# Optimization experiments

Measured on AMD Instinct MI355X. Metric: run time of the kernel, lower is better.

The kernel has to match this reference:

```python
import jax, jax.numpy as jnp
import numpy as np

N, NFEAT, NHID, NREL, NCLASS, NHEADS = 4096, 512, 64, 64, 16, 8
ALPHA = 0.2   # LeakyReLU negative slope
NEG = -9e15   # pyGAT mask value


def _gat_layer(x, rel, mask, adj_ad, W, a1, a2, concat):
    # x: [N, Fin], rel: [nrel, Fin], mask: [N, N] bool, adj_ad: [N, nrel]
    xr = x + adj_ad @ rel                 # relation-augmented node features
    h = xr @ W                            # [N, Fout]
    f1 = h @ a1                           # [N]  (a^T[Wh_i||Wh_j] = f1_i + f2_j)
    f2 = h @ a2                           # [N]
    e = jax.nn.leaky_relu(f1[:, None] + f2[None, :], ALPHA)  # [N, N]
    att = jax.nn.softmax(jnp.where(mask, e, NEG), axis=1)
    out = att @ h                         # [N, Fout]
    return jax.nn.elu(out) if concat else out


def setup_inputs() -> dict:
    key = jax.random.key(0)
    ks = jax.random.split(key, 12)
    x = jax.random.normal(ks[0], (N, NFEAT), jnp.float32)
    rel = jax.random.normal(ks[1], (NREL, NFEAT), jnp.float32)
    rel_dict = jax.random.randint(ks[2], (N,), 0, NREL, jnp.int32)
    adj = (jax.random.uniform(ks[3], (N, N)) < 0.01).astype(jnp.float32)
    adj = jnp.maximum(adj, jnp.eye(N, dtype=jnp.float32))  # self loops
    adj_ad = jax.random.uniform(ks[4], (N, NREL), jnp.float32)
    adj_ad = adj_ad / adj_ad.sum(axis=1, keepdims=True)
    s_in = 1.0 / np.sqrt(NFEAT)
    s_hid = 1.0 / np.sqrt(NHID)
    s_cat = 1.0 / np.sqrt(NHID * NHEADS)
    W_heads = jax.random.normal(ks[5], (NHEADS, NFEAT, NHID), jnp.float32) * s_in
    a1_heads = jax.random.normal(ks[6], (NHEADS, NHID), jnp.float32) * s_hid
    a2_heads = jax.random.normal(ks[7], (NHEADS, NHID), jnp.float32) * s_hid
    W_out = jax.random.normal(ks[8], (NHID * NHEADS, NFEAT), jnp.float32) * s_cat
    a1_out = jax.random.normal(ks[9], (NFEAT,), jnp.float32) * s_in
    a2_out = jax.random.normal(ks[10], (NFEAT,), jnp.float32) * s_in
    lin_W = jax.random.normal(ks[11], (NFEAT, NCLASS), jnp.float32) * s_in
    lin_b = jnp.zeros((NCLASS,), jnp.float32)
    return {"x": x, "rel": rel, "rel_dict": rel_dict, "adj": adj, "adj_ad": adj_ad,
            "W_heads": W_heads, "a1_heads": a1_heads, "a2_heads": a2_heads,
            "W_out": W_out, "a1_out": a1_out, "a2_out": a2_out,
            "lin_W": lin_W, "lin_b": lin_b}


def reference(x, rel, rel_dict, adj, adj_ad, W_heads, a1_heads, a2_heads,
              W_out, a1_out, a2_out, lin_W, lin_b):
    # dropout is identity at inference (training=False); rel_dict is only used
    # by the repo to build adj/adj_ad, so it is a non-math constant here.
    mask = adj > 0
    # multi-head GAT layer, heads fused via vmap then concatenated on feature dim
    heads = jax.vmap(lambda W, a1, a2: _gat_layer(x, rel, mask, adj_ad, W, a1, a2, True))(
        W_heads, a1_heads, a2_heads)                      # [H, N, NHID]
    hcat = jnp.moveaxis(heads, 0, 1).reshape(N, NHEADS * NHID)  # [N, H*NHID]
    h2 = _gat_layer(hcat, rel, mask, adj_ad, W_out, a1_out, a2_out, False)  # [N, NFEAT]
    logits = jax.nn.elu(h2 @ lin_W + lin_b)               # [N, NCLASS]
    return jax.nn.log_softmax(logits, axis=1)
```

## Files before the change

kernel.cpp:

```cpp
#include <hip/hip_runtime.h>

#define NN      4096
#define FEAT    512
#define NHID    64
#define NHEADS  8
#define NCLS    16
#define MAXDEG  128
#define ALPHA   0.2f

typedef __bf16 bf16_t;
typedef __bf16 bf16x8_t __attribute__((ext_vector_type(8)));
typedef float  f32x4_t  __attribute__((ext_vector_type(4)));
typedef unsigned short us8_t __attribute__((ext_vector_type(8)));

__device__ inline unsigned short f2bf(float f) {
    unsigned int u = __float_as_uint(f);
    u += 0x7fffu + ((u >> 16) & 1u);
    return (unsigned short)(u >> 16);
}
__device__ inline float bfu2f(unsigned short b) {
    return __uint_as_float(((unsigned int)b) << 16);
}

__global__ __launch_bounds__(128) void rmmfuse_kernel(
    const float* __restrict__ adj_ad, const float* __restrict__ rel,
    const float* __restrict__ x, float* __restrict__ R,
    bf16_t* __restrict__ Abf) {
    int i = blockIdx.x;
    int t = threadIdx.x;
    __shared__ float sa[64];
    if (t < 64) sa[t] = adj_ad[i * 64 + t];
    __syncthreads();
    float4 acc = make_float4(0.f, 0.f, 0.f, 0.f);
    for (int r = 0; r < 64; ++r) {
        float a = sa[r];
        float4 rv = ((const float4*)(rel + r * FEAT))[t];
        acc.x += a * rv.x; acc.y += a * rv.y;
        acc.z += a * rv.z; acc.w += a * rv.w;
    }
    ((float4*)(R + (size_t)i * FEAT))[t] = acc;
    float4 xv = ((const float4*)(x + (size_t)i * FEAT))[t];
    ushort4 o;
    o.x = f2bf(acc.x + xv.x); o.y = f2bf(acc.y + xv.y);
    o.z = f2bf(acc.z + xv.z); o.w = f2bf(acc.w + xv.w);
    *(ushort4*)(Abf + (size_t)i * FEAT + 4 * t) = o;
}

__global__ __launch_bounds__(256) void wperm_kernel(
    const float* __restrict__ Wh, const float* __restrict__ Wo,
    unsigned short* __restrict__ WcT, unsigned short* __restrict__ WoT) {
    int gid = blockIdx.x * 256 + threadIdx.x;
    if (gid < 262144) {
        int idx = gid;
        int n = idx >> 9, k = idx & 511;
        int h = n >> 6, f = n & 63;
        WcT[idx] = f2bf(Wh[(h * 512 + k) * 64 + f]);
    } else {
        int idx = gid - 262144;
        int n = idx >> 9, k = idx & 511;
        WoT[idx] = f2bf(Wo[k * 512 + n]);
    }
}

__global__ __launch_bounds__(256) void gemm_bf16_dot_kernel(
    const bf16_t* __restrict__ A, const bf16_t* __restrict__ Bt,
    unsigned short* __restrict__ Cbf,
    const float* __restrict__ a1, const float* __restrict__ a2,
    float* __restrict__ f1, float* __restrict__ f2, int layer2) {
    __shared__ __align__(16) bf16_t As[64][72];
    __shared__ __align__(16) bf16_t Bs[64][72];
    const int bm = blockIdx.x * 64;
    const int bn = blockIdx.y * 64;
    const int t  = threadIdx.x;
    const int lr = t >> 3;
    const int lc = (t & 7) * 8;
    const int l  = t & 63;
    const int w  = t >> 6;
    const int mrow = w * 16 + (l & 15);
    const int nrow = l & 15;
    const int q8 = (l >> 4) * 8;

    f32x4_t acc[4] = {};
    for (int k0 = 0; k0 < FEAT; k0 += 64) {
        *(uint4*)&As[lr][lc]      = *(const uint4*)(A  + (size_t)(bm + lr)      * FEAT + k0 + lc);
        *(uint4*)&As[32 + lr][lc] = *(const uint4*)(A  + (size_t)(bm + 32 + lr) * FEAT + k0 + lc);
        *(uint4*)&Bs[lr][lc]      = *(const uint4*)(Bt + (size_t)(bn + lr)      * FEAT + k0 + lc);
        *(uint4*)&Bs[32 + lr][lc] = *(const uint4*)(Bt + (size_t)(bn + 32 + lr) * FEAT + k0 + lc);
        __syncthreads();
        #pragma unroll
        for (int kk = 0; kk < 64; kk += 32) {
            bf16x8_t a = *(const bf16x8_t*)&As[mrow][kk + q8];
            #pragma unroll
            for (int nt = 0; nt < 4; ++nt) {
                bf16x8_t b = *(const bf16x8_t*)&Bs[nt * 16 + nrow][kk + q8];
                acc[nt] = __builtin_amdgcn_mfma_f32_16x16x32_bf16(a, b, acc[nt], 0, 0, 0);
            }
        }
        __syncthreads();
    }
    const int crow = bm + w * 16 + (l >> 4) * 4;
    const int ccol = bn + (l & 15);
    #pragma unroll
    for (int nt = 0; nt < 4; ++nt)
        #pragma unroll
        for (int r = 0; r < 4; ++r)
            Cbf[(size_t)(crow + r) * FEAT + ccol + nt * 16] = f2bf(acc[nt][r]);

    float a1v[4], a2v[4];
    #pragma unroll
    for (int nt = 0; nt < 4; ++nt) {
        a1v[nt] = a1[bn + (l & 15) + nt * 16];
        a2v[nt] = a2[bn + (l & 15) + nt * 16];
    }
    float p1[4] = {}, p2[4] = {};
    #pragma unroll
    for (int nt = 0; nt < 4; ++nt)
        #pragma unroll
        for (int r = 0; r < 4; ++r) {
            p1[r] += acc[nt][r] * a1v[nt];
            p2[r] += acc[nt][r] * a2v[nt];
        }
    #pragma unroll
    for (int off = 1; off <= 8; off <<= 1)
        #pragma unroll
        for (int r = 0; r < 4; ++r) {
            p1[r] += __shfl_xor(p1[r], off);
            p2[r] += __shfl_xor(p2[r], off);
        }
    if ((l & 15) == 0) {
        int row = bm + w * 16 + (l >> 4) * 4;
        if (layer2) {
            #pragma unroll
            for (int r = 0; r < 4; ++r) {
                atomicAdd(&f1[row + r], p1[r]);
                atomicAdd(&f2[row + r], p2[r]);
            }
        } else {
            #pragma unroll
            for (int r = 0; r < 4; ++r) {
                f1[blockIdx.y * NN + row + r] = p1[r];
                f2[blockIdx.y * NN + row + r] = p2[r];
            }
        }
    }
}

__global__ __launch_bounds__(256) void initf_kernel(float* __restrict__ f1o,
                                                    float* __restrict__ f2o) {
    int idx = blockIdx.x * 256 + threadIdx.x;
    ((float4*)f1o)[idx] = make_float4(0.f, 0.f, 0.f, 0.f);
    ((float4*)f2o)[idx] = make_float4(0.f, 0.f, 0.f, 0.f);
}

__device__ inline void csr_emit(unsigned long long m, int lane, int* cnt,
                                int* colrow, int j) {
    if (m) {
        int tot = __popcll(m);
        int base = 0;
        if (lane == 0) base = atomicAdd(cnt, tot);
        base = __shfl(base, 0);
        if (m & (1ULL << lane)) {
            int pos = __popcll(m & ((1ULL << lane) - 1));
            int idx = base + pos;
            if (idx < MAXDEG) colrow[idx] = j;
        }
    }
}
__global__ __launch_bounds__(256) void csr_kernel(
    const float* __restrict__ adj, int* __restrict__ deg, int* __restrict__ cols) {
    int i = blockIdx.x;
    int t = threadIdx.x;
    int lane = t & 63;
    __shared__ int cnt;
    if (t == 0) cnt = 0;
    __syncthreads();
    const float4* row4 = (const float4*)(adj + (size_t)i * NN);
    int* colrow = cols + i * MAXDEG;
    for (int j4 = t; j4 < NN / 4; j4 += 256) {
        float4 v = row4[j4];
        int j = j4 * 4;
        csr_emit(__ballot(v.x > 0.0f), lane, &cnt, colrow, j);
        csr_emit(__ballot(v.y > 0.0f), lane, &cnt, colrow, j + 1);
        csr_emit(__ballot(v.z > 0.0f), lane, &cnt, colrow, j + 2);
        csr_emit(__ballot(v.w > 0.0f), lane, &cnt, colrow, j + 3);
    }
    __syncthreads();
    if (t == 0) deg[i] = cnt > MAXDEG ? MAXDEG : cnt;
}

__global__ __launch_bounds__(512) void att1_kernel(
    const bf16_t* __restrict__ Hbf, const float* __restrict__ f1,
    const float* __restrict__ f2, const int* __restrict__ deg,
    const int* __restrict__ cols, const float* __restrict__ R,
    bf16_t* __restrict__ outbf) {
    int i = blockIdx.x;
    int h = threadIdx.x >> 6;
    int l = threadIdx.x & 63;
    __shared__ int jl[MAXDEG];
    __shared__ float se[NHEADS][MAXDEG];
    __shared__ int sdeg;
    if (threadIdx.x == 0) sdeg = deg[i];
    __syncthreads();
    int d = sdeg;
    int dpad = (d + 15) & ~15;
    for (int k = threadIdx.x; k < dpad; k += 512)
        jl[k] = (k < d) ? cols[i * MAXDEG + k] : i;
    __syncthreads();
    float fi = f1[h * NN + i];
    float lmax = -1e30f;
    for (int k = l; k < d; k += 64) {
        float e = fi + f2[h * NN + jl[k]];
        e = e > 0.0f ? e : ALPHA * e;
        se[h][k] = e;
        lmax = fmaxf(lmax, e);
    }
    for (int off = 32; off; off >>= 1) lmax = fmaxf(lmax, __shfl_down(lmax, off));
    float m = __shfl(lmax, 0);
    float ls = 0.0f;
    for (int k = l; k < d; k += 64) {
        float p = __expf(se[h][k] - m);
        se[h][k] = p;
        ls += p;
    }
    for (int k = d + l; k < dpad; k += 64) se[h][k] = 0.0f;
    for (int off = 32; off; off >>= 1) ls += __shfl_down(ls, off);
    float s = __shfl(ls, 0);
    const int slot = l >> 3;
    const int cg   = l & 7;
    float acc[8] = {};
    for (int k0 = 0; k0 < dpad; k0 += 16) {
        int ka = k0 + slot;
        int kb = k0 + 8 + slot;
        float pa = se[h][ka];
        us8_t va = *(const us8_t*)(Hbf + (size_t)jl[ka] * FEAT + h * 64 + cg * 8);
        float pb = (kb < dpad) ? se[h][kb] : 0.0f;
        us8_t vb = (kb < dpad) ? *(const us8_t*)(Hbf + (size_t)jl[kb] * FEAT + h * 64 + cg * 8)
                               : va;
        #pragma unroll
        for (int j = 0; j < 8; ++j) acc[j] += pa * bfu2f(va[j]);
        #pragma unroll
        for (int j = 0; j < 8; ++j) acc[j] += pb * bfu2f(vb[j]);
    }
    #pragma unroll
    for (int off = 8; off <= 32; off <<= 1)
        #pragma unroll
        for (int j = 0; j < 8; ++j) acc[j] += __shfl_xor(acc[j], off);
    if (slot == 0) {
        float inv = 1.0f / s;
        const float* Rrow = R + (size_t)i * FEAT + h * 64 + cg * 8;
        float4 r0 = *(const float4*)(Rrow);
        float4 r1 = *(const float4*)(Rrow + 4);
        float o[8];
        #pragma unroll
        for (int j = 0; j < 8; ++j) {
            float v = acc[j] * inv;
            o[j] = v > 0.0f ? v : __expf(v) - 1.0f;
        }
        o[0] += r0.x; o[1] += r0.y; o[2] += r0.z; o[3] += r0.w;
        o[4] += r1.x; o[5] += r1.y; o[6] += r1.z; o[7] += r1.w;
        ushort4 pk0, pk1;
        pk0.x = f2bf(o[0]); pk0.y = f2bf(o[1]); pk0.z = f2bf(o[2]); pk0.w = f2bf(o[3]);
        pk1.x = f2bf(o[4]); pk1.y = f2bf(o[5]); pk1.z = f2bf(o[6]); pk1.w = f2bf(o[7]);
        ushort4* dst = (ushort4*)(outbf + (size_t)i * FEAT + h * 64 + cg * 8);
        dst[0] = pk0;
        dst[1] = pk1;
    }
}

__global__ __launch_bounds__(256) void att2_final_kernel(
    const bf16_t* __restrict__ Hbf, const float* __restrict__ f1,
    const float* __restrict__ f2, const int* __restrict__ deg,
    const int* __restrict__ cols, const float* __restrict__ linW,
    const float* __restrict__ linb, float* __restrict__ out) {
    int i = blockIdx.x;
    int t = threadIdx.x;
    __shared__ int jl[MAXDEG];
    __shared__ float sp[MAXDEG];
    __shared__ float red[4];
    __shared__ float part[3][FEAT];
    __shared__ float hrow[FEAT];
    __shared__ float clsred[16][NCLS];
    __shared__ float sl[NCLS];
    __shared__ int sdeg;
    if (t == 0) sdeg = deg[i];
    __syncthreads();
    int d = sdeg;
    int dpad = (d + 7) & ~7;
    if (t < dpad) jl[t] = (t < d) ? cols[i * MAXDEG + t] : i;
    __syncthreads();
    float e = 0.0f, lmax = -1e30f;
    if (t < d) {
        e = f1[i] + f2[jl[t]];
        e = e > 0.0f ? e : ALPHA * e;
        lmax = e;
    }
    for (int off = 32; off; off >>= 1) lmax = fmaxf(lmax, __shfl_down(lmax, off));
    if ((t & 63) == 0) red[t >> 6] = lmax;
    __syncthreads();
    float m = fmaxf(fmaxf(red[0], red[1]), fmaxf(red[2], red[3]));
    float p = 0.0f;
    if (t < d) p = __expf(e - m);
    if (t < dpad) sp[t] = p;
    float ls = p;
    for (int off = 32; off; off >>= 1) ls += __shfl_down(ls, off);
    __syncthreads();
    if ((t & 63) == 0) red[t >> 6] = ls;
    __syncthreads();
    float s = red[0] + red[1] + red[2] + red[3];
    float inv = 1.0f / s;
    const int slot = t >> 6;
    const int cg   = t & 63;
    float acc[8] = {};
    for (int k0 = 0; k0 < dpad; k0 += 8) {
        int ka = k0 + slot;
        int kb = k0 + 4 + slot;
        float pa = sp[ka];
        us8_t va = *(const us8_t*)(Hbf + (size_t)jl[ka] * FEAT + cg * 8);
        float pb = (kb < dpad) ? sp[kb] : 0.0f;
        us8_t vb = (kb < dpad) ? *(const us8_t*)(Hbf + (size_t)jl[kb] * FEAT + cg * 8) : va;
        #pragma unroll
        for (int j = 0; j < 8; ++j) acc[j] += pa * bfu2f(va[j]);
        #pragma unroll
        for (int j = 0; j < 8; ++j) acc[j] += pb * bfu2f(vb[j]);
    }
    if (slot > 0) {
        float* dst = &part[slot - 1][cg * 8];
        *(float4*)(dst)     = make_float4(acc[0], acc[1], acc[2], acc[3]);
        *(float4*)(dst + 4) = make_float4(acc[4], acc[5], acc[6], acc[7]);
    }
    __syncthreads();
    if (slot == 0) {
        #pragma unroll
        for (int sl2 = 0; sl2 < 3; ++sl2)
            #pragma unroll
            for (int j = 0; j < 8; ++j) acc[j] += part[sl2][cg * 8 + j];
        float* dst = &hrow[cg * 8];
        *(float4*)(dst)     = make_float4(acc[0] * inv, acc[1] * inv, acc[2] * inv, acc[3] * inv);
        *(float4*)(dst + 4) = make_float4(acc[4] * inv, acc[5] * inv, acc[6] * inv, acc[7] * inv);
    }
    __syncthreads();
    {
        int c = t & 15;
        int seg = t >> 4;
        float partial = 0.0f;
        int f0 = seg * 32;
        #pragma unroll 8
        for (int f = f0; f < f0 + 32; ++f) partial += hrow[f] * linW[f * NCLS + c];
        clsred[seg][c] = partial;
    }
    __syncthreads();
    if (t < NCLS) {
        float logit = linb[t];
        #pragma unroll
        for (int seg = 0; seg < 16; ++seg) logit += clsred[seg][t];
        logit = logit > 0.0f ? logit : __expf(logit) - 1.0f;
        sl[t] = logit;
    }
    __syncthreads();
    if (t < NCLS) {
        float mm = sl[0];
        #pragma unroll
        for (int c = 1; c < NCLS; ++c) mm = fmaxf(mm, sl[c]);
        float ssum = 0.0f;
        #pragma unroll
        for (int c = 0; c < NCLS; ++c) ssum += __expf(sl[c] - mm);
        out[i * NCLS + t] = sl[t] - mm - logf(ssum);
    }
}

extern "C" void kernel_launch(void* const* d_in, const int* in_sizes, int n_in,
                              void* d_out, int out_size, void* d_ws, size_t ws_size,
                              hipStream_t stream) {
    const float* x        = (const float*)d_in[0];
    const float* rel      = (const float*)d_in[1];
    const float* adj      = (const float*)d_in[3];
    const float* adj_ad   = (const float*)d_in[4];
    const float* W_heads  = (const float*)d_in[5];
    const float* a1_heads = (const float*)d_in[6];
    const float* a2_heads = (const float*)d_in[7];
    const float* W_out    = (const float*)d_in[8];
    const float* a1_out   = (const float*)d_in[9];
    const float* a2_out   = (const float*)d_in[10];
    const float* lin_W    = (const float*)d_in[11];
    const float* lin_b    = (const float*)d_in[12];
    float* out = (float*)d_out;

    char* ws = (char*)d_ws;
    bf16_t* Abf  = (bf16_t*)(ws);
    bf16_t* Abf2 = (bf16_t*)(ws + (4u  << 20));
    bf16_t* Hbf1 = (bf16_t*)(ws + (8u  << 20));
    bf16_t* Hbf2 = (bf16_t*)(ws + (12u << 20));
    float*  R    = (float*) (ws + (16u << 20));
    bf16_t* WcT  = (bf16_t*)(ws + (24u << 20));
    bf16_t* WoT  = (bf16_t*)(ws + (24u << 20) + (512u << 10));
    float*  f1   = (float*) (ws + (25u << 20));
    float*  f2   = (float*) (ws + (25u << 20) + (128u << 10));
    float*  f1o  = (float*) (ws + (25u << 20) + (256u << 10));
    float*  f2o  = (float*) (ws + (25u << 20) + (272u << 10));
    int*    deg  = (int*)   (ws + (25u << 20) + (288u << 10));
    int*    cols = (int*)   (ws + (26u << 20));

    csr_kernel<<<NN, 256, 0, stream>>>(adj, deg, cols);
    rmmfuse_kernel<<<NN, 128, 0, stream>>>(adj_ad, rel, x, R, Abf);
    wperm_kernel<<<2048, 256, 0, stream>>>(W_heads, W_out, (unsigned short*)WcT, (unsigned short*)WoT);
    gemm_bf16_dot_kernel<<<dim3(64, 8), 256, 0, stream>>>(
        Abf, WcT, (unsigned short*)Hbf1, a1_heads, a2_heads, f1, f2, 0);
    att1_kernel<<<NN, 512, 0, stream>>>(Hbf1, f1, f2, deg, cols, R, Abf2);
    initf_kernel<<<4, 256, 0, stream>>>(f1o, f2o);
    gemm_bf16_dot_kernel<<<dim3(64, 8), 256, 0, stream>>>(
        Abf2, WoT, (unsigned short*)Hbf2, a1_out, a2_out, f1o, f2o, 1);
    att2_final_kernel<<<NN, 256, 0, stream>>>(Hbf2, f1o, f2o, deg, cols, lin_W, lin_b, out);
}
```

Baseline: 223.1 us.

## Restructure attention gathers to full-row loads and fold f-init into weight permute

```diff
diff --git a/kernel.cpp b/kernel.cpp
--- a/kernel.cpp
+++ b/kernel.cpp
@@ -48,17 +48,22 @@
 
 __global__ __launch_bounds__(256) void wperm_kernel(
     const float* __restrict__ Wh, const float* __restrict__ Wo,
-    unsigned short* __restrict__ WcT, unsigned short* __restrict__ WoT) {
+    unsigned short* __restrict__ WcT, unsigned short* __restrict__ WoT,
+    float* __restrict__ f1o, float* __restrict__ f2o) {
     int gid = blockIdx.x * 256 + threadIdx.x;
     if (gid < 262144) {
         int idx = gid;
         int n = idx >> 9, k = idx & 511;
         int h = n >> 6, f = n & 63;
         WcT[idx] = f2bf(Wh[(h * 512 + k) * 64 + f]);
-    } else {
+    } else if (gid < 524288) {
         int idx = gid - 262144;
         int n = idx >> 9, k = idx & 511;
         WoT[idx] = f2bf(Wo[k * 512 + n]);
+    } else {
+        int idx = gid - 524288;
+        ((float4*)f1o)[idx] = make_float4(0.f, 0.f, 0.f, 0.f);
+        ((float4*)f2o)[idx] = make_float4(0.f, 0.f, 0.f, 0.f);
     }
 }
 
@@ -145,13 +150,6 @@
     }
 }
 
-__global__ __launch_bounds__(256) void initf_kernel(float* __restrict__ f1o,
-                                                    float* __restrict__ f2o) {
-    int idx = blockIdx.x * 256 + threadIdx.x;
-    ((float4*)f1o)[idx] = make_float4(0.f, 0.f, 0.f, 0.f);
-    ((float4*)f2o)[idx] = make_float4(0.f, 0.f, 0.f, 0.f);
-}
-
 __device__ inline void csr_emit(unsigned long long m, int lane, int* cnt,
                                 int* colrow, int j) {
     if (m) {
@@ -194,16 +192,19 @@
     const int* __restrict__ cols, const float* __restrict__ R,
     bf16_t* __restrict__ outbf) {
     int i = blockIdx.x;
-    int h = threadIdx.x >> 6;
-    int l = threadIdx.x & 63;
+    int tid = threadIdx.x;
+    int h = tid >> 6;
+    int l = tid & 63;
     __shared__ int jl[MAXDEG];
     __shared__ float se[NHEADS][MAXDEG];
+    __shared__ float part[NHEADS][FEAT];
+    __shared__ float sinv[NHEADS];
     __shared__ int sdeg;
-    if (threadIdx.x == 0) sdeg = deg[i];
+    if (tid == 0) sdeg = deg[i];
     __syncthreads();
     int d = sdeg;
-    int dpad = (d + 15) & ~15;
-    for (int k = threadIdx.x; k < dpad; k += 512)
+    int dpad = (d + 31) & ~31;
+    for (int k = tid; k < dpad; k += 512)
         jl[k] = (k < d) ? cols[i * MAXDEG + k] : i;
     __syncthreads();
     float fi = f1[h * NN + i];
@@ -224,46 +225,38 @@
     }
     for (int k = d + l; k < dpad; k += 64) se[h][k] = 0.0f;
     for (int off = 32; off; off >>= 1) ls += __shfl_down(ls, off);
-    float s = __shfl(ls, 0);
-    const int slot = l >> 3;
-    const int cg   = l & 7;
+    if (l == 0) sinv[h] = 1.0f / ls;
+    __syncthreads();
+    const int myhead = l >> 3;
     float acc[8] = {};
-    for (int k0 = 0; k0 < dpad; k0 += 16) {
-        int ka = k0 + slot;
-        int kb = k0 + 8 + slot;
-        float pa = se[h][ka];
-        us8_t va = *(const us8_t*)(Hbf + (size_t)jl[ka] * FEAT + h * 64 + cg * 8);
-        float pb = (kb < dpad) ? se[h][kb] : 0.0f;
-        us8_t vb = (kb < dpad) ? *(const us8_t*)(Hbf + (size_t)jl[kb] * FEAT + h * 64 + cg * 8)
-                               : va;
-        #pragma unroll
-        for (int j = 0; j < 8; ++j) acc[j] += pa * bfu2f(va[j]);
-        #pragma unroll
-        for (int j = 0; j < 8; ++j) acc[j] += pb * bfu2f(vb[j]);
-    }
-    #pragma unroll
-    for (int off = 8; off <= 32; off <<= 1)
-        #pragma unroll
-        for (int j = 0; j < 8; ++j) acc[j] += __shfl_xor(acc[j], off);
-    if (slot == 0) {
-        float inv = 1.0f / s;
-        const float* Rrow = R + (size_t)i * FEAT + h * 64 + cg * 8;
-        float4 r0 = *(const float4*)(Rrow);
-        float4 r1 = *(const float4*)(Rrow + 4);
-        float o[8];
-        #pragma unroll
-        for (int j = 0; j < 8; ++j) {
-            float v = acc[j] * inv;
-            o[j] = v > 0.0f ? v : __expf(v) - 1.0f;
-        }
-        o[0] += r0.x; o[1] += r0.y; o[2] += r0.z; o[3] += r0.w;
-        o[4] += r1.x; o[5] += r1.y; o[6] += r1.z; o[7] += r1.w;
-        ushort4 pk0, pk1;
-        pk0.x = f2bf(o[0]); pk0.y = f2bf(o[1]); pk0.z = f2bf(o[2]); pk0.w = f2bf(o[3]);
-        pk1.x = f2bf(o[4]); pk1.y = f2bf(o[5]); pk1.z = f2bf(o[6]); pk1.w = f2bf(o[7]);
-        ushort4* dst = (ushort4*)(outbf + (size_t)i * FEAT + h * 64 + cg * 8);
-        dst[0] = pk0;
-        dst[1] = pk1;
+    for (int k0 = 0; k0 < dpad; k0 += 32) {
+        float pw[4];
+        const bf16_t* rp[4];
+        #pragma unroll
+        for (int j = 0; j < 4; ++j) {
+            int k = k0 + j * 8 + h;
+            pw[j] = se[myhead][k];
+            rp[j] = Hbf + (size_t)jl[k] * FEAT + l * 8;
+        }
+        #pragma unroll
+        for (int j = 0; j < 4; ++j) {
+            us8_t v = *(const us8_t*)rp[j];
+            float p = pw[j];
+            #pragma unroll
+            for (int q = 0; q < 8; ++q) acc[q] += p * bfu2f(v[q]);
+        }
+    }
+    *(float4*)&part[h][l * 8]     = make_float4(acc[0], acc[1], acc[2], acc[3]);
+    *(float4*)&part[h][l * 8 + 4] = make_float4(acc[4], acc[5], acc[6], acc[7]);
+    __syncthreads();
+    {
+        float sum = 0.0f;
+        #pragma unroll
+        for (int w2 = 0; w2 < NHEADS; ++w2) sum += part[w2][tid];
+        float o = sum * sinv[tid >> 6];
+        o = o > 0.0f ? o : __expf(o) - 1.0f;
+        o += R[(size_t)i * FEAT + tid];
+        ((unsigned short*)outbf)[(size_t)i * FEAT + tid] = f2bf(o);
     }
 }
 
@@ -285,7 +278,7 @@
     if (t == 0) sdeg = deg[i];
     __syncthreads();
     int d = sdeg;
-    int dpad = (d + 7) & ~7;
+    int dpad = (d + 15) & ~15;
     if (t < dpad) jl[t] = (t < d) ? cols[i * MAXDEG + t] : i;
     __syncthreads();
     float e = 0.0f, lmax = -1e30f;
@@ -311,17 +304,22 @@
     const int slot = t >> 6;
     const int cg   = t & 63;
     float acc[8] = {};
-    for (int k0 = 0; k0 < dpad; k0 += 8) {
-        int ka = k0 + slot;
-        int kb = k0 + 4 + slot;
-        float pa = sp[ka];
-        us8_t va = *(const us8_t*)(Hbf + (size_t)jl[ka] * FEAT + cg * 8);
-        float pb = (kb < dpad) ? sp[kb] : 0.0f;
-        us8_t vb = (kb < dpad) ? *(const us8_t*)(Hbf + (size_t)jl[kb] * FEAT + cg * 8) : va;
-        #pragma unroll
-        for (int j = 0; j < 8; ++j) acc[j] += pa * bfu2f(va[j]);
-        #pragma unroll
-        for (int j = 0; j < 8; ++j) acc[j] += pb * bfu2f(vb[j]);
+    for (int k0 = 0; k0 < dpad; k0 += 16) {
+        float pw[4];
+        const bf16_t* rp[4];
+        #pragma unroll
+        for (int j = 0; j < 4; ++j) {
+            int k = k0 + j * 4 + slot;
+            pw[j] = sp[k];
+            rp[j] = Hbf + (size_t)jl[k] * FEAT + cg * 8;
+        }
+        #pragma unroll
+        for (int j = 0; j < 4; ++j) {
+            us8_t v = *(const us8_t*)rp[j];
+            float pk = pw[j];
+            #pragma unroll
+            for (int q = 0; q < 8; ++q) acc[q] += pk * bfu2f(v[q]);
+        }
     }
     if (slot > 0) {
         float* dst = &part[slot - 1][cg * 8];
@@ -402,11 +400,11 @@
 
     csr_kernel<<<NN, 256, 0, stream>>>(adj, deg, cols);
     rmmfuse_kernel<<<NN, 128, 0, stream>>>(adj_ad, rel, x, R, Abf);
-    wperm_kernel<<<2048, 256, 0, stream>>>(W_heads, W_out, (unsigned short*)WcT, (unsigned short*)WoT);
+    wperm_kernel<<<2052, 256, 0, stream>>>(W_heads, W_out,
+        (unsigned short*)WcT, (unsigned short*)WoT, f1o, f2o);
     gemm_bf16_dot_kernel<<<dim3(64, 8), 256, 0, stream>>>(
         Abf, WcT, (unsigned short*)Hbf1, a1_heads, a2_heads, f1, f2, 0);
     att1_kernel<<<NN, 512, 0, stream>>>(Hbf1, f1, f2, deg, cols, R, Abf2);
-    initf_kernel<<<4, 256, 0, stream>>>(f1o, f2o);
     gemm_bf16_dot_kernel<<<dim3(64, 8), 256, 0, stream>>>(
         Abf2, WoT, (unsigned short*)Hbf2, a1_out, a2_out, f1o, f2o, 1);
     att2_final_kernel<<<NN, 256, 0, stream>>>(Hbf2, f1o, f2o, deg, cols, lin_W, lin_b, out);
```

Result: faster. 215.9 us (-3.2%).
